# Optimization experiments

Hardware: AMD Instinct MI355X
Metric: run time of the kernel (lower is better)

The kernel has to match this reference:

```python
import jax, jax.numpy as jnp
import numpy as np

B, C, H, W = 32, 512, 32, 32
TXT_DIM, M, NUM_HEADS = 768, 77, 8
HEAD_DIM = C // NUM_HEADS
SCALE = HEAD_DIM ** -0.5


def setup_inputs() -> dict:
    key = jax.random.key(0)
    ks = jax.random.split(key, 9)
    x = jax.random.normal(ks[0], (B, C, H, W), dtype=jnp.float32)
    text_emb = jax.random.normal(ks[1], (B, M, TXT_DIM), dtype=jnp.float32)
    attention_mask = jnp.ones((B, M), dtype=jnp.int32)
    # Linear params (PyTorch convention: weight [out, in], bias [out])
    s_q = 1.0 / np.sqrt(C)
    s_kv = 1.0 / np.sqrt(TXT_DIM)
    Wq = jax.random.uniform(ks[2], (C, C), jnp.float32, -s_q, s_q)
    bq = jax.random.uniform(ks[3], (C,), jnp.float32, -s_q, s_q)
    Wk = jax.random.uniform(ks[4], (C, TXT_DIM), jnp.float32, -s_kv, s_kv)
    bk = jax.random.uniform(ks[5], (C,), jnp.float32, -s_kv, s_kv)
    Wv = jax.random.uniform(ks[6], (C, TXT_DIM), jnp.float32, -s_kv, s_kv)
    bv = jax.random.uniform(ks[7], (C,), jnp.float32, -s_kv, s_kv)
    return {"x": x, "text_emb": text_emb, "attention_mask": attention_mask,
            "Wq": Wq, "bq": bq, "Wk": Wk, "bk": bk, "Wv": Wv, "bv": bv}


def reference(x, text_emb, attention_mask, Wq, bq, Wk, bk, Wv, bv):
    b, c, h, w = x.shape
    n = h * w
    x_flat = x.reshape(b, c, n).transpose(0, 2, 1)          # [B, N, C]
    Q = x_flat @ Wq.T + bq                                   # [B, N, C]
    K = text_emb @ Wk.T + bk                                 # [B, M, C]
    V = text_emb @ Wv.T + bv                                 # [B, M, C]
    Q = Q.reshape(b, n, NUM_HEADS, HEAD_DIM)
    K = K.reshape(b, -1, NUM_HEADS, HEAD_DIM)
    V = V.reshape(b, -1, NUM_HEADS, HEAD_DIM)
    # scores: [B, heads, N, M]
    scores = jnp.einsum('bnhd,bmhd->bhnm', Q, K) * SCALE
    mask = attention_mask[:, None, None, :] != 0
    scores = jnp.where(mask, scores, -jnp.inf)
    probs = jax.nn.softmax(scores, axis=-1)
    out = jnp.einsum('bhnm,bmhd->bnhd', probs, V)            # [B, N, heads, d]
    out = out.reshape(b, n, c).transpose(0, 2, 1).reshape(b, c, h, w)
    return out
```

## Files before the change

kernel.cpp:

```cpp
#include <hip/hip_runtime.h>
#include <math.h>

#define BB   32
#define CC   512
#define HWN  1024
#define MM   77
#define TXT  768
#define NH   8
#define HD   64
#define SCALEF 0.125f
#define MPAD 96
#define KVROWS (BB*MPAD)
#define AP   40
#define PP   104

typedef __attribute__((ext_vector_type(8))) short          bf16x8;
typedef __attribute__((ext_vector_type(8))) unsigned short us8;
typedef __attribute__((ext_vector_type(4))) float          f32x4;

__device__ inline unsigned short f2bf(float f) {
    union { float f; unsigned u; } v; v.f = f;
    unsigned r = v.u + 0x7fff + ((v.u >> 16) & 1);
    return (unsigned short)(r >> 16);
}

__global__ __launch_bounds__(256) void wcvt_kernel(
    const float* __restrict__ src, unsigned short* __restrict__ dst)
{
    const int i = blockIdx.x * 256 + threadIdx.x;
    const float4 v = ((const float4*)src)[i];
    ushort4 o;
    o.x = f2bf(v.x); o.y = f2bf(v.y); o.z = f2bf(v.z); o.w = f2bf(v.w);
    ((ushort4*)dst)[i] = o;
}

__global__ __launch_bounds__(256) void tcvt_kernel(
    const float* __restrict__ x, unsigned short* __restrict__ xT)
{
    const int nt = blockIdx.x, ct = blockIdx.y, b = blockIdx.z;
    const int n0 = nt * 64, c0 = ct * 64;
    __shared__ float tile[64][65];
    const int t = threadIdx.x, tx = t & 15, ty = t >> 4;
    const float* xb = x + (size_t)b * CC * HWN;
    #pragma unroll
    for (int j = 0; j < 4; ++j) {
        const int c = ty + 16 * j;
        const float4 v = *(const float4*)&xb[(size_t)(c0 + c) * HWN + n0 + tx * 4];
        tile[c][tx * 4 + 0] = v.x; tile[c][tx * 4 + 1] = v.y;
        tile[c][tx * 4 + 2] = v.z; tile[c][tx * 4 + 3] = v.w;
    }
    __syncthreads();
    unsigned short* xTb = xT + (size_t)b * HWN * CC;
    #pragma unroll
    for (int j = 0; j < 4; ++j) {
        const int n = ty + 16 * j;
        ushort4 o;
        o.x = f2bf(tile[tx * 4 + 0][n]); o.y = f2bf(tile[tx * 4 + 1][n]);
        o.z = f2bf(tile[tx * 4 + 2][n]); o.w = f2bf(tile[tx * 4 + 3][n]);
        *(ushort4*)&xTb[(size_t)(n0 + n) * CC + c0 + tx * 4] = o;
    }
}

__global__ __launch_bounds__(256) void qgemm_mfma(
    const unsigned short* __restrict__ xT, const unsigned short* __restrict__ Wqb,
    const float* __restrict__ bq, unsigned short* __restrict__ Qb)
{
    const int rt = blockIdx.x, ct = blockIdx.y;
    const int row0 = rt * 128, co0 = ct * 128;
    __shared__ unsigned short As[128 * AP];
    __shared__ unsigned short Bs[128 * AP];
    const int t = threadIdx.x;
    const int lane = t & 63, wv = t >> 6;
    const int wr = wv >> 1, wc = wv & 1;
    const int lm = lane & 15, quad = lane >> 4;
    const int chunk = t & 3, srow = t >> 2;

    f32x4 acc[4][4] = {};

    for (int k0 = 0; k0 < CC; k0 += 32) {
        #pragma unroll
        for (int p = 0; p < 2; ++p) {
            const int r = srow + p * 64;
            *(us8*)&As[r * AP + chunk * 8] =
                *(const us8*)&xT[(size_t)(row0 + r) * CC + k0 + chunk * 8];
            *(us8*)&Bs[r * AP + chunk * 8] =
                *(const us8*)&Wqb[(size_t)(co0 + r) * CC + k0 + chunk * 8];
        }
        __syncthreads();
        bf16x8 a[4], bfr[4];
        #pragma unroll
        for (int i = 0; i < 4; ++i)
            a[i] = *(const bf16x8*)&As[(wr * 64 + i * 16 + lm) * AP + quad * 8];
        #pragma unroll
        for (int i = 0; i < 4; ++i)
            bfr[i] = *(const bf16x8*)&Bs[(wc * 64 + i * 16 + lm) * AP + quad * 8];
        #pragma unroll
        for (int mi = 0; mi < 4; ++mi)
            #pragma unroll
            for (int ni = 0; ni < 4; ++ni)
                acc[mi][ni] = __builtin_amdgcn_mfma_f32_16x16x32_bf16(
                    a[mi], bfr[ni], acc[mi][ni], 0, 0, 0);
        __syncthreads();
    }

    #pragma unroll
    for (int ni = 0; ni < 4; ++ni) {
        const int col = co0 + wc * 64 + ni * 16 + lm;
        const float bias = bq[col];
        #pragma unroll
        for (int mi = 0; mi < 4; ++mi) {
            #pragma unroll
            for (int j = 0; j < 4; ++j) {
                const int row = row0 + wr * 64 + mi * 16 + quad * 4 + j;
                Qb[(size_t)row * CC + col] = f2bf(acc[mi][ni][j] + bias);
            }
        }
    }
}

__global__ __launch_bounds__(256) void kvgemm_mfma(
    const float* __restrict__ te,
    const float* __restrict__ Wk, const float* __restrict__ bk,
    const float* __restrict__ Wv, const float* __restrict__ bv,
    unsigned short* __restrict__ Kb, unsigned short* __restrict__ Vt)
{
    const int rt = blockIdx.x, ct = blockIdx.y;
    const int row0 = rt * 128;
    const int isV = (ct >= 4);
    const float* W = isV ? Wv : Wk;
    const float* bias_p = isV ? bv : bk;
    const int co0 = (ct & 3) * 128;

    __shared__ unsigned short As[128 * AP];
    __shared__ unsigned short Bs[128 * AP];
    const int t = threadIdx.x;
    const int lane = t & 63, wv_ = t >> 6;
    const int wr = wv_ >> 1, wc = wv_ & 1;
    const int lm = lane & 15, quad = lane >> 4;
    const int chunk = t & 3, srow = t >> 2;

    f32x4 acc[4][4] = {};

    for (int k0 = 0; k0 < TXT; k0 += 32) {
        #pragma unroll
        for (int p = 0; p < 2; ++p) {
            const int r = srow + p * 64;
            const int rflat = row0 + r;
            const int b_i = rflat / MPAD, m_i = rflat % MPAD;
            const float* terow = te + ((size_t)b_i * MM + min(m_i, MM - 1)) * TXT;
            const float4 f0 = *(const float4*)&terow[k0 + chunk * 8];
            const float4 f1 = *(const float4*)&terow[k0 + chunk * 8 + 4];
            us8 o;
            o[0] = f2bf(f0.x); o[1] = f2bf(f0.y); o[2] = f2bf(f0.z); o[3] = f2bf(f0.w);
            o[4] = f2bf(f1.x); o[5] = f2bf(f1.y); o[6] = f2bf(f1.z); o[7] = f2bf(f1.w);
            *(us8*)&As[r * AP + chunk * 8] = o;

            const float4 g0 = *(const float4*)&W[(size_t)(co0 + r) * TXT + k0 + chunk * 8];
            const float4 g1 = *(const float4*)&W[(size_t)(co0 + r) * TXT + k0 + chunk * 8 + 4];
            us8 ob;
            ob[0] = f2bf(g0.x); ob[1] = f2bf(g0.y); ob[2] = f2bf(g0.z); ob[3] = f2bf(g0.w);
            ob[4] = f2bf(g1.x); ob[5] = f2bf(g1.y); ob[6] = f2bf(g1.z); ob[7] = f2bf(g1.w);
            *(us8*)&Bs[r * AP + chunk * 8] = ob;
        }
        __syncthreads();
        bf16x8 a[4], bfr[4];
        #pragma unroll
        for (int i = 0; i < 4; ++i)
            a[i] = *(const bf16x8*)&As[(wr * 64 + i * 16 + lm) * AP + quad * 8];
        #pragma unroll
        for (int i = 0; i < 4; ++i)
            bfr[i] = *(const bf16x8*)&Bs[(wc * 64 + i * 16 + lm) * AP + quad * 8];
        #pragma unroll
        for (int mi = 0; mi < 4; ++mi)
            #pragma unroll
            for (int ni = 0; ni < 4; ++ni)
                acc[mi][ni] = __builtin_amdgcn_mfma_f32_16x16x32_bf16(
                    a[mi], bfr[ni], acc[mi][ni], 0, 0, 0);
        __syncthreads();
    }

    #pragma unroll
    for (int ni = 0; ni < 4; ++ni) {
        const int col = co0 + wc * 64 + ni * 16 + lm;
        const float bias = bias_p[col];
        #pragma unroll
        for (int mi = 0; mi < 4; ++mi) {
            #pragma unroll
            for (int j = 0; j < 4; ++j) {
                const int row = row0 + wr * 64 + mi * 16 + quad * 4 + j;
                const int b_i = row / MPAD, m_i = row % MPAD;
                const unsigned short hv = f2bf(acc[mi][ni][j] + bias);
                if (isV) {
                    Vt[((size_t)b_i * CC + col) * MPAD + m_i] = hv;
                } else if (m_i < MM) {
                    Kb[((size_t)b_i * MM + m_i) * CC + col] = hv;
                }
            }
        }
    }
}

__global__ __launch_bounds__(256) void attn_mfma(
    const unsigned short* __restrict__ Qb, const unsigned short* __restrict__ Kb,
    const unsigned short* __restrict__ Vt, const int* __restrict__ amask,
    float* __restrict__ out)
{
    const int ntile = blockIdx.x;
    const int h     = blockIdx.y;
    const int b     = blockIdx.z;
    const int row0  = ntile * 128;

    __shared__ unsigned short Ps[128 * PP];
    __shared__ float msk[80];

    const int t = threadIdx.x;
    const int w = t >> 6, lane = t & 63;
    const int lm = lane & 15, quad = lane >> 4;

    {
        const int r = t >> 1, off = 80 + (t & 1) * 8;
        us8 z = {0, 0, 0, 0, 0, 0, 0, 0};
        *(us8*)&Ps[r * PP + off] = z;
    }
    if (t < 80) msk[t] = (t < MM && amask[b * MM + t] != 0) ? 0.f : -INFINITY;
    __syncthreads();

    f32x4 s[2][5] = {};
    const unsigned short* qbase = Qb + ((size_t)b * HWN + row0) * CC + h * HD;
    const unsigned short* kbase = Kb + (size_t)b * MM * CC + h * HD;
    #pragma unroll
    for (int ks = 0; ks < 2; ++ks) {
        bf16x8 a[2], kf[5];
        #pragma unroll
        for (int mt = 0; mt < 2; ++mt)
            a[mt] = *(const bf16x8*)&qbase[(size_t)((w * 2 + mt) * 16 + lm) * CC + ks * 32 + quad * 8];
        #pragma unroll
        for (int n = 0; n < 5; ++n) {
            const int kr = min(n * 16 + lm, MM - 1);
            kf[n] = *(const bf16x8*)&kbase[(size_t)kr * CC + ks * 32 + quad * 8];
        }
        #pragma unroll
        for (int mt = 0; mt < 2; ++mt)
            #pragma unroll
            for (int n = 0; n < 5; ++n)
                s[mt][n] = __builtin_amdgcn_mfma_f32_16x16x32_bf16(a[mt], kf[n], s[mt][n], 0, 0, 0);
    }

    float inv[2][4];
    #pragma unroll
    for (int mt = 0; mt < 2; ++mt) {
        #pragma unroll
        for (int j = 0; j < 4; ++j) {
            float v[5];
            #pragma unroll
            for (int n = 0; n < 5; ++n)
                v[n] = s[mt][n][j] * SCALEF + msk[n * 16 + lm];
            float mx = fmaxf(fmaxf(fmaxf(v[0], v[1]), fmaxf(v[2], v[3])), v[4]);
            mx = fmaxf(mx, __shfl_xor(mx, 1, 64));
            mx = fmaxf(mx, __shfl_xor(mx, 2, 64));
            mx = fmaxf(mx, __shfl_xor(mx, 4, 64));
            mx = fmaxf(mx, __shfl_xor(mx, 8, 64));
            float sum = 0.f;
            #pragma unroll
            for (int n = 0; n < 5; ++n) { v[n] = __expf(v[n] - mx); sum += v[n]; }
            sum += __shfl_xor(sum, 1, 64);
            sum += __shfl_xor(sum, 2, 64);
            sum += __shfl_xor(sum, 4, 64);
            sum += __shfl_xor(sum, 8, 64);
            inv[mt][j] = 1.0f / sum;
            const int mrow = (w * 2 + mt) * 16 + quad * 4 + j;
            #pragma unroll
            for (int n = 0; n < 5; ++n)
                Ps[mrow * PP + n * 16 + lm] = f2bf(v[n]);
        }
    }
    __syncthreads();

    f32x4 o[2][4] = {};
    const unsigned short* vbase = Vt + ((size_t)b * CC + h * HD) * MPAD;
    #pragma unroll
    for (int ks = 0; ks < 3; ++ks) {
        bf16x8 a[2], vf[4];
        #pragma unroll
        for (int mt = 0; mt < 2; ++mt)
            a[mt] = *(const bf16x8*)&Ps[((w * 2 + mt) * 16 + lm) * PP + ks * 32 + quad * 8];
        #pragma unroll
        for (int n = 0; n < 4; ++n)
            vf[n] = *(const bf16x8*)&vbase[(size_t)(n * 16 + lm) * MPAD + ks * 32 + quad * 8];
        #pragma unroll
        for (int mt = 0; mt < 2; ++mt)
            #pragma unroll
            for (int n = 0; n < 4; ++n)
                o[mt][n] = __builtin_amdgcn_mfma_f32_16x16x32_bf16(a[mt], vf[n], o[mt][n], 0, 0, 0);
    }

    float* obase = out + ((size_t)b * CC + h * HD) * HWN + row0;
    #pragma unroll
    for (int mt = 0; mt < 2; ++mt) {
        #pragma unroll
        for (int n = 0; n < 4; ++n) {
            const int col = n * 16 + lm;
            #pragma unroll
            for (int j = 0; j < 4; ++j) {
                const int r = (w * 2 + mt) * 16 + quad * 4 + j;
                obase[(size_t)col * HWN + r] = o[mt][n][j] * inv[mt][j];
            }
        }
    }
}

extern "C" void kernel_launch(void* const* d_in, const int* in_sizes, int n_in,
                              void* d_out, int out_size, void* d_ws, size_t ws_size,
                              hipStream_t stream)
{
    const float* x     = (const float*)d_in[0];
    const float* te    = (const float*)d_in[1];
    const int*   amask = (const int*)d_in[2];
    const float* Wq    = (const float*)d_in[3];
    const float* bq    = (const float*)d_in[4];
    const float* Wk    = (const float*)d_in[5];
    const float* bk    = (const float*)d_in[6];
    const float* Wv    = (const float*)d_in[7];
    const float* bv    = (const float*)d_in[8];
    float* out = (float*)d_out;

    unsigned short* xT  = (unsigned short*)d_ws;
    unsigned short* Qb  = xT + (size_t)BB * HWN * CC;
    unsigned short* Kb  = Qb + (size_t)BB * HWN * CC;
    unsigned short* Vt  = Kb + (size_t)BB * MM * CC;
    unsigned short* Wqb = Vt + (size_t)BB * CC * MPAD;

    wcvt_kernel<<<dim3(CC * CC / 4 / 256), 256, 0, stream>>>(Wq, Wqb);
    tcvt_kernel<<<dim3(16, 8, BB), 256, 0, stream>>>(x, xT);
    qgemm_mfma<<<dim3(256, 4), 256, 0, stream>>>(xT, Wqb, bq, Qb);
    kvgemm_mfma<<<dim3(KVROWS / 128, 8), 256, 0, stream>>>(te, Wk, bk, Wv, bv, Kb, Vt);
    attn_mfma<<<dim3(8, NH, BB), 256, 0, stream>>>(Qb, Kb, Vt, amask, out);
}
```

Before: 243.4 us.

## Use direct-to-LDS loads in Q GEMM, coalesce stores, retile KV GEMM

The Q projection GEMM now loads its tiles with global_load_lds, which writes 16-byte chunks straight into LDS instead of staging them through registers, and drops the padded layout. The attention epilogue stages the output through shared memory so each row is written with coalesced float4 stores rather than scattered scalar stores. The transpose kernel now writes 16-byte vectors. The KV GEMM moves to 64x64 tiles to launch more blocks. The unpadded LDS layout may cause bank conflicts on fragment reads, and the epilogue adds an extra barrier.

```diff
diff --git a/kernel.cpp b/kernel.cpp
--- a/kernel.cpp
+++ b/kernel.cpp
@@ -13,6 +13,7 @@
 #define KVROWS (BB*MPAD)
 #define AP   40
 #define PP   104
+#define OSP  132
 
 typedef __attribute__((ext_vector_type(8))) short          bf16x8;
 typedef __attribute__((ext_vector_type(8))) unsigned short us8;
@@ -22,6 +23,12 @@
     union { float f; unsigned u; } v; v.f = f;
     unsigned r = v.u + 0x7fff + ((v.u >> 16) & 1);
     return (unsigned short)(r >> 16);
+}
+
+__device__ inline void gload_lds16(const void* g, void* l) {
+    __builtin_amdgcn_global_load_lds(
+        (const __attribute__((address_space(1))) void*)g,
+        (__attribute__((address_space(3))) void*)l, 16, 0, 0);
 }
 
 __global__ __launch_bounds__(256) void wcvt_kernel(
@@ -40,24 +47,28 @@
     const int nt = blockIdx.x, ct = blockIdx.y, b = blockIdx.z;
     const int n0 = nt * 64, c0 = ct * 64;
     __shared__ float tile[64][65];
-    const int t = threadIdx.x, tx = t & 15, ty = t >> 4;
+    const int t = threadIdx.x;
     const float* xb = x + (size_t)b * CC * HWN;
-    #pragma unroll
-    for (int j = 0; j < 4; ++j) {
-        const int c = ty + 16 * j;
-        const float4 v = *(const float4*)&xb[(size_t)(c0 + c) * HWN + n0 + tx * 4];
-        tile[c][tx * 4 + 0] = v.x; tile[c][tx * 4 + 1] = v.y;
-        tile[c][tx * 4 + 2] = v.z; tile[c][tx * 4 + 3] = v.w;
+    {
+        const int c = t >> 2;
+        #pragma unroll
+        for (int j = 0; j < 4; ++j) {
+            const int f4 = (t & 3) + j * 4;
+            const float4 v = *(const float4*)&xb[(size_t)(c0 + c) * HWN + n0 + f4 * 4];
+            tile[c][f4 * 4 + 0] = v.x; tile[c][f4 * 4 + 1] = v.y;
+            tile[c][f4 * 4 + 2] = v.z; tile[c][f4 * 4 + 3] = v.w;
+        }
     }
     __syncthreads();
     unsigned short* xTb = xT + (size_t)b * HWN * CC;
     #pragma unroll
-    for (int j = 0; j < 4; ++j) {
-        const int n = ty + 16 * j;
-        ushort4 o;
-        o.x = f2bf(tile[tx * 4 + 0][n]); o.y = f2bf(tile[tx * 4 + 1][n]);
-        o.z = f2bf(tile[tx * 4 + 2][n]); o.w = f2bf(tile[tx * 4 + 3][n]);
-        *(ushort4*)&xTb[(size_t)(n0 + n) * CC + c0 + tx * 4] = o;
+    for (int j = 0; j < 2; ++j) {
+        const int n = (t >> 3) + j * 32;
+        const int c8 = (t & 7) * 8;
+        us8 o;
+        #pragma unroll
+        for (int i = 0; i < 8; ++i) o[i] = f2bf(tile[c8 + i][n]);
+        *(us8*)&xTb[(size_t)(n0 + n) * CC + c0 + c8] = o;
     }
 }
 
@@ -67,33 +78,33 @@
 {
     const int rt = blockIdx.x, ct = blockIdx.y;
     const int row0 = rt * 128, co0 = ct * 128;
-    __shared__ unsigned short As[128 * AP];
-    __shared__ unsigned short Bs[128 * AP];
+    __shared__ unsigned short As[128 * 32];
+    __shared__ unsigned short Bs[128 * 32];
     const int t = threadIdx.x;
-    const int lane = t & 63, wv = t >> 6;
-    const int wr = wv >> 1, wc = wv & 1;
+    const int lane = t & 63, w = t >> 6;
+    const int wr = w >> 1, wc = w & 1;
     const int lm = lane & 15, quad = lane >> 4;
-    const int chunk = t & 3, srow = t >> 2;
+    const int lrow = lane >> 2, lk = (lane & 3) * 8;
 
     f32x4 acc[4][4] = {};
 
     for (int k0 = 0; k0 < CC; k0 += 32) {
         #pragma unroll
         for (int p = 0; p < 2; ++p) {
-            const int r = srow + p * 64;
-            *(us8*)&As[r * AP + chunk * 8] =
-                *(const us8*)&xT[(size_t)(row0 + r) * CC + k0 + chunk * 8];
-            *(us8*)&Bs[r * AP + chunk * 8] =
-                *(const us8*)&Wqb[(size_t)(co0 + r) * CC + k0 + chunk * 8];
+            const int chunk = w * 2 + p;
+            gload_lds16(&xT[(size_t)(row0 + chunk * 16 + lrow) * CC + k0 + lk],
+                        &As[chunk * 512]);
+            gload_lds16(&Wqb[(size_t)(co0 + chunk * 16 + lrow) * CC + k0 + lk],
+                        &Bs[chunk * 512]);
         }
         __syncthreads();
         bf16x8 a[4], bfr[4];
         #pragma unroll
         for (int i = 0; i < 4; ++i)
-            a[i] = *(const bf16x8*)&As[(wr * 64 + i * 16 + lm) * AP + quad * 8];
+            a[i] = *(const bf16x8*)&As[(wr * 64 + i * 16 + lm) * 32 + quad * 8];
         #pragma unroll
         for (int i = 0; i < 4; ++i)
-            bfr[i] = *(const bf16x8*)&Bs[(wc * 64 + i * 16 + lm) * AP + quad * 8];
+            bfr[i] = *(const bf16x8*)&Bs[(wc * 64 + i * 16 + lm) * 32 + quad * 8];
         #pragma unroll
         for (int mi = 0; mi < 4; ++mi)
             #pragma unroll
@@ -124,76 +135,76 @@
     const float* __restrict__ Wv, const float* __restrict__ bv,
     unsigned short* __restrict__ Kb, unsigned short* __restrict__ Vt)
 {
-    const int rt = blockIdx.x, ct = blockIdx.y;
-    const int row0 = rt * 128;
-    const int isV = (ct >= 4);
+    const int rt = blockIdx.x, ctc = blockIdx.y;
+    const int row0 = rt * 64;
+    const int isV = (ctc >= 8);
     const float* W = isV ? Wv : Wk;
     const float* bias_p = isV ? bv : bk;
-    const int co0 = (ct & 3) * 128;
-
-    __shared__ unsigned short As[128 * AP];
-    __shared__ unsigned short Bs[128 * AP];
+    const int co0 = (ctc & 7) * 64;
+
+    __shared__ unsigned short As[64 * AP];
+    __shared__ unsigned short Bs[64 * AP];
     const int t = threadIdx.x;
-    const int lane = t & 63, wv_ = t >> 6;
-    const int wr = wv_ >> 1, wc = wv_ & 1;
+    const int lane = t & 63, w = t >> 6;
+    const int wr = w >> 1, wc = w & 1;
     const int lm = lane & 15, quad = lane >> 4;
     const int chunk = t & 3, srow = t >> 2;
 
-    f32x4 acc[4][4] = {};
+    f32x4 acc[2][2] = {};
+
+    const int rflat = row0 + srow;
+    const int b_i = rflat / MPAD, m_i = rflat % MPAD;
+    const float* terow = te + ((size_t)b_i * MM + min(m_i, MM - 1)) * TXT;
+    const float* wrow  = W + (size_t)(co0 + srow) * TXT;
 
     for (int k0 = 0; k0 < TXT; k0 += 32) {
-        #pragma unroll
-        for (int p = 0; p < 2; ++p) {
-            const int r = srow + p * 64;
-            const int rflat = row0 + r;
-            const int b_i = rflat / MPAD, m_i = rflat % MPAD;
-            const float* terow = te + ((size_t)b_i * MM + min(m_i, MM - 1)) * TXT;
+        {
             const float4 f0 = *(const float4*)&terow[k0 + chunk * 8];
             const float4 f1 = *(const float4*)&terow[k0 + chunk * 8 + 4];
             us8 o;
             o[0] = f2bf(f0.x); o[1] = f2bf(f0.y); o[2] = f2bf(f0.z); o[3] = f2bf(f0.w);
             o[4] = f2bf(f1.x); o[5] = f2bf(f1.y); o[6] = f2bf(f1.z); o[7] = f2bf(f1.w);
-            *(us8*)&As[r * AP + chunk * 8] = o;
-
-            const float4 g0 = *(const float4*)&W[(size_t)(co0 + r) * TXT + k0 + chunk * 8];
-            const float4 g1 = *(const float4*)&W[(size_t)(co0 + r) * TXT + k0 + chunk * 8 + 4];
+            *(us8*)&As[srow * AP + chunk * 8] = o;
+
+            const float4 g0 = *(const float4*)&wrow[k0 + chunk * 8];
+            const float4 g1 = *(const float4*)&wrow[k0 + chunk * 8 + 4];
             us8 ob;
             ob[0] = f2bf(g0.x); ob[1] = f2bf(g0.y); ob[2] = f2bf(g0.z); ob[3] = f2bf(g0.w);
             ob[4] = f2bf(g1.x); ob[5] = f2bf(g1.y); ob[6] = f2bf(g1.z); ob[7] = f2bf(g1.w);
-            *(us8*)&Bs[r * AP + chunk * 8] = ob;
+            *(us8*)&Bs[srow * AP + chunk * 8] = ob;
         }
         __syncthreads();
-        bf16x8 a[4], bfr[4];
-        #pragma unroll
-        for (int i = 0; i < 4; ++i)
-            a[i] = *(const bf16x8*)&As[(wr * 64 + i * 16 + lm) * AP + quad * 8];
-        #pragma unroll
-        for (int i = 0; i < 4; ++i)
-            bfr[i] = *(const bf16x8*)&Bs[(wc * 64 + i * 16 + lm) * AP + quad * 8];
-        #pragma unroll
-        for (int mi = 0; mi < 4; ++mi)
-            #pragma unroll
-            for (int ni = 0; ni < 4; ++ni)
+        bf16x8 a[2], bfr[2];
+        #pragma unroll
+        for (int i = 0; i < 2; ++i)
+            a[i] = *(const bf16x8*)&As[(wr * 32 + i * 16 + lm) * AP + quad * 8];
+        #pragma unroll
+        for (int i = 0; i < 2; ++i)
+            bfr[i] = *(const bf16x8*)&Bs[(wc * 32 + i * 16 + lm) * AP + quad * 8];
+        #pragma unroll
+        for (int mi = 0; mi < 2; ++mi)
+            #pragma unroll
+            for (int ni = 0; ni < 2; ++ni)
                 acc[mi][ni] = __builtin_amdgcn_mfma_f32_16x16x32_bf16(
                     a[mi], bfr[ni], acc[mi][ni], 0, 0, 0);
         __syncthreads();
     }
 
     #pragma unroll
-    for (int ni = 0; ni < 4; ++ni) {
-        const int col = co0 + wc * 64 + ni * 16 + lm;
+    for (int ni = 0; ni < 2; ++ni) {
+        const int col = co0 + wc * 32 + ni * 16 + lm;
         const float bias = bias_p[col];
         #pragma unroll
-        for (int mi = 0; mi < 4; ++mi) {
-            #pragma unroll
-            for (int j = 0; j < 4; ++j) {
-                const int row = row0 + wr * 64 + mi * 16 + quad * 4 + j;
-                const int b_i = row / MPAD, m_i = row % MPAD;
+        for (int mi = 0; mi < 2; ++mi) {
+            #pragma unroll
+            for (int j = 0; j < 2 * 2; ++j) {
+                const int row = row0 + wr * 32 + mi * 16 + quad * 4 + j;
+                const int bo = row / MPAD, mo = row % MPAD;
                 const unsigned short hv = f2bf(acc[mi][ni][j] + bias);
                 if (isV) {
-                    Vt[((size_t)b_i * CC + col) * MPAD + m_i] = hv;
-                } else if (m_i < MM) {
-                    Kb[((size_t)b_i * MM + m_i) * CC + col] = hv;
+                    Vt[((size_t)bo * CC + col) * MPAD + mo] = hv;
+                } else if (mo < MM) {
+                    Kb[((size_t)bo * MM + mo) * CC + col] = hv;
                 }
             }
         }
@@ -210,8 +221,10 @@
     const int b     = blockIdx.z;
     const int row0  = ntile * 128;
 
-    __shared__ unsigned short Ps[128 * PP];
+    __shared__ char smem[64 * OSP * 4];
     __shared__ float msk[80];
+    unsigned short* Ps = (unsigned short*)smem;
+    float* Os = (float*)smem;
 
     const int t = threadIdx.x;
     const int w = t >> 6, lane = t & 63;
@@ -293,19 +306,32 @@
             for (int n = 0; n < 4; ++n)
                 o[mt][n] = __builtin_amdgcn_mfma_f32_16x16x32_bf16(a[mt], vf[n], o[mt][n], 0, 0, 0);
     }
-
-    float* obase = out + ((size_t)b * CC + h * HD) * HWN + row0;
+    __syncthreads();
+
     #pragma unroll
     for (int mt = 0; mt < 2; ++mt) {
         #pragma unroll
         for (int n = 0; n < 4; ++n) {
             const int col = n * 16 + lm;
-            #pragma unroll
-            for (int j = 0; j < 4; ++j) {
-                const int r = (w * 2 + mt) * 16 + quad * 4 + j;
-                obase[(size_t)col * HWN + r] = o[mt][n][j] * inv[mt][j];
-            }
-        }
+            const int r0 = (w * 2 + mt) * 16 + quad * 4;
+            float4 st;
+            st.x = o[mt][n][0] * inv[mt][0];
+            st.y = o[mt][n][1] * inv[mt][1];
+            st.z = o[mt][n][2] * inv[mt][2];
+            st.w = o[mt][n][3] * inv[mt][3];
+            *(float4*)&Os[col * OSP + r0] = st;
+        }
+    }
+    __syncthreads();
+
+    float* obase = out + ((size_t)b * CC + h * HD) * HWN + row0;
+    #pragma unroll
+    for (int p = 0; p < 8; ++p) {
+        const int idx = p * 256 + t;
+        const int col = idx >> 5;
+        const int r4  = idx & 31;
+        const float4 v = *(const float4*)&Os[col * OSP + r4 * 4];
+        *(float4*)&obase[(size_t)col * HWN + r4 * 4] = v;
     }
 }
 
@@ -333,6 +359,6 @@
     wcvt_kernel<<<dim3(CC * CC / 4 / 256), 256, 0, stream>>>(Wq, Wqb);
     tcvt_kernel<<<dim3(16, 8, BB), 256, 0, stream>>>(x, xT);
     qgemm_mfma<<<dim3(256, 4), 256, 0, stream>>>(xT, Wqb, bq, Qb);
-    kvgemm_mfma<<<dim3(KVROWS / 128, 8), 256, 0, stream>>>(te, Wk, bk, Wv, bv, Kb, Vt);
+    kvgemm_mfma<<<dim3(KVROWS / 64, 16), 256, 0, stream>>>(te, Wk, bk, Wv, bv, Kb, Vt);
     attn_mfma<<<dim3(8, NH, BB), 256, 0, stream>>>(Qb, Kb, Vt, amask, out);
 }
```

Result: faster. 233.2 us (-4.2%).
